# Kernel tuning notes

Hardware: AMD Instinct MI355X
Metric: run time of the kernel (lower is better)

The kernel has to match this reference:

```python
import jax, jax.numpy as jnp
import numpy as np

# AWLoss config (matches init_kwargs): method='fft', filter_dim=2, filter_scale=2,
# mode='reverse', reduction='sum', epsilon=1e-9 (pre-whitening), std=1e-4, eta=0, gamma=0
EPSILON = 1e-9
STD = 1e-4
DIMS = (-2, -1)          # self.dims for filter_dim=2
FS = (3, 511, 511)       # get_filter_shape([B,3,256,256]): [nc, 2H-1, 2W-1]


def pad_signal(x, shape):
    # center-pad dims 1.. of x up to `shape` (extra sample on the right).
    pads = [(0, 0)]
    for i, s in enumerate(shape):
        p1 = (s - x.shape[i + 1]) // 2
        pads.append((p1, s - x.shape[i + 1] - p1))
    return jnp.pad(x, pads)


def make_penalty(shape, std):
    # inverted multivariate gaussian on [-1,1]^d grid: 0 at center, ->1 away
    axes = [jnp.linspace(-1.0, 1.0, n) for n in shape]
    mesh = jnp.stack(jnp.meshgrid(*axes, indexing='ij'), axis=-1)  # (h, w, 2)
    d = mesh.shape[-1]
    logp = -0.5 * jnp.sum((mesh / std) ** 2, axis=-1) \
           - 0.5 * d * jnp.log(2.0 * jnp.pi * std * std)
    rv = jnp.exp(logp)
    rv = rv / jnp.max(jnp.abs(rv))
    return -rv + jnp.max(rv)  # eta=0 => no random additive term


def wienerfft(x, y, fs, prwh):
    # least-squares Wiener filter transforming x into y, via FFT
    Fx_flip = jnp.fft.fftn(jnp.flip(x, DIMS), axes=DIMS)
    Fccorr = Fx_flip * jnp.fft.fftn(y, axes=DIMS)   # cross-correlation spectrum
    Facorr = Fx_flip * jnp.fft.fftn(x, axes=DIMS)   # auto-correlation spectrum
    Fdconv = (Fccorr + prwh) / (Facorr + prwh)      # regularized deconvolution
    # irfftn crops last axis to fs[-1]//2+1 (numpy/torch semantics match)
    rolled = jnp.fft.irfftn(Fdconv, s=fs[-2:], axes=DIMS)
    # roll: int(-n/2)-1 per trailing dim (n odd => -(n//2)-1)
    shifts = tuple(-(x.shape[i] // 2) - 1 for i in range(1, x.ndim))[-2:]
    return jnp.roll(rolled, shifts, axis=DIMS)


def awloss(recon, target):
    fs = FS
    recon_p = pad_signal(recon, fs)   # [B, C, 511, 511]
    target_p = pad_signal(target, fs)
    # mode='reverse': filter transforms target into recon
    x, y = target_p, recon_p
    v = wienerfft(x, y, fs, EPSILON)                       # [B, C, 511, 511]
    vnorm = jnp.sqrt(jnp.sum(v * v, axis=DIMS, keepdims=True))
    v = v / vnorm                                          # unit-energy filter
    T = make_penalty(fs[-2:], STD)                         # (511, 511)
    f = 0.5 * jnp.sum((T * v) ** 2)                        # reduction='sum'
    return f


def setup_inputs() -> dict:
    key = jax.random.key(0)
    k1, k2 = jax.random.split(key)
    recon = jax.random.normal(k1, (16, 3, 256, 256), dtype=jnp.float32)
    target = jax.random.normal(k2, (16, 3, 256, 256), dtype=jnp.float32)
    return {"recon": recon, "target": target}


def reference(recon, target):
    return awloss(recon, target)
```

## Files before the change

### kernel.cpp

```cpp
#include <hip/hip_runtime.h>
#include <math.h>


#define NCH 48
#define PADOFF 127
#define TWO_PI_F 6.283185307179586f

typedef float f32x4 __attribute__((ext_vector_type(4)));
typedef short s16x8 __attribute__((ext_vector_type(8)));
typedef unsigned short u16;

typedef __attribute__((address_space(1))) const unsigned char* gas_p;
typedef __attribute__((address_space(3))) unsigned char* las_p;

union frag_u { u16 u[8]; s16x8 v; };

__device__ __forceinline__ u16 f2bf(float f) {
    union { float f; unsigned u; } x; x.f = f;
    unsigned r = x.u + 0x7FFFu + ((x.u >> 16) & 1u);
    return (u16)(r >> 16);
}

#define MFMA16(A, B, C) __builtin_amdgcn_mfma_f32_16x16x32_bf16(A, B, C, 0, 0, 0)

__global__ __launch_bounds__(256) void setup(u16* __restrict__ w2f,
                                             float* __restrict__ sacc) {
    __shared__ float cs[511], sn[511];
    int tid = threadIdx.x;
    for (int i = tid; i < 511; i += 256) {
        float a = -TWO_PI_F * (float)i / 511.0f;
        cs[i] = cosf(a);
        sn[i] = sinf(a);
    }
    __syncthreads();

    int i = blockIdx.x * 256 + tid;
    int j = i & 7, l = (i >> 3) & 63, kk = (i >> 9) & 7;
    int c = (i >> 12) & 1, kt = i >> 13;
    int k1 = 16 * kt + (l & 15);
    u16 v = 0;
    if (k1 < 511) {
        int n = 32 * kk + 8 * (l >> 4) + j;
        int p = (k1 * (n + PADOFF)) % 511;
        v = f2bf(c ? sn[p] : cs[p]);
    }
    w2f[i] = v;
    if (blockIdx.x == 0 && tid < 2 * NCH) sacc[tid] = 0.0f;
}

__global__ __launch_bounds__(256, 2) void stage1(const float* __restrict__ target,
                                                 const float* __restrict__ recon,
                                                 const u16* __restrict__ w2f,
                                                 u16* __restrict__ x1t,
                                                 int c0) {
    int tid = threadIdx.x;
    int w = tid >> 6, l = tid & 63;
    int lm = l & 15, lh = l >> 4;
    int h   = blockIdx.x & 1;
    int q   = (blockIdx.x >> 1) & 3;
    int imgl = blockIdx.x >> 3;
    int lc = imgl >> 1;
    int tsel = imgl & 1;
    const float* src = (tsel == 0 ? target : recon) + (size_t)(c0 + lc) * 65536;
    int r0 = 64 * q;

    __shared__ u16 lin[16384];

    {
        int row = tid >> 2;
        int cg  = tid & 3;
        const float* rp = src + (size_t)(r0 + row) * 256 + cg * 64;
        float4 v[16];
        #pragma unroll
        for (int i = 0; i < 16; ++i) v[i] = *(const float4*)(rp + 4 * i);
        u16 b[64];
        #pragma unroll
        for (int i = 0; i < 16; ++i) {
            b[4*i]   = f2bf(v[i].x); b[4*i+1] = f2bf(v[i].y);
            b[4*i+2] = f2bf(v[i].z); b[4*i+3] = f2bf(v[i].w);
        }
        int s = row >> 4, lmw = row & 15;
        #pragma unroll
        for (int i2 = 0; i2 < 8; ++i2) {
            int col0 = cg * 64 + i2 * 8;
            int kk = col0 >> 5, lhw = (col0 >> 3) & 3;
            u16* dst = &lin[((s * 8 + kk) * 512) + (lhw * 16 + lmw) * 8];
            *(s16x8*)dst = *(const s16x8*)&b[i2 * 8];
        }
    }

    int t0 = 8 * h + 2 * w;
    s16x8 tw00[8], tw01[8], tw10[8], tw11[8];
    {
        const u16* p0 = w2f + (size_t)t0 * 8192 + l * 8;
        const u16* p1 = w2f + (size_t)(t0 + 1) * 8192 + l * 8;
        #pragma unroll
        for (int kk = 0; kk < 8; ++kk) {
            tw00[kk] = *(const s16x8*)(p0 + kk * 512);
            tw01[kk] = *(const s16x8*)(p0 + 4096 + kk * 512);
            tw10[kk] = *(const s16x8*)(p1 + kk * 512);
            tw11[kk] = *(const s16x8*)(p1 + 4096 + kk * 512);
        }
    }
    __syncthreads();

    f32x4 a00[4], a01[4], a10[4], a11[4];
    #pragma unroll
    for (int s = 0; s < 4; ++s) {
        a00[s] = (f32x4){0,0,0,0}; a01[s] = (f32x4){0,0,0,0};
        a10[s] = (f32x4){0,0,0,0}; a11[s] = (f32x4){0,0,0,0};
    }
    #pragma unroll
    for (int kk = 0; kk < 8; ++kk) {
        s16x8 af[4];
        #pragma unroll
        for (int s = 0; s < 4; ++s)
            af[s] = *(const s16x8*)&lin[((s * 8 + kk) * 512) + l * 8];
        #pragma unroll
        for (int s = 0; s < 4; ++s) {
            a00[s] = MFMA16(af[s], tw00[kk], a00[s]);
            a01[s] = MFMA16(af[s], tw01[kk], a01[s]);
            a10[s] = MFMA16(af[s], tw10[kk], a10[s]);
            a11[s] = MFMA16(af[s], tw11[kk], a11[s]);
        }
    }

    u16* chdst = x1t + (size_t)(lc * 4 + tsel * 2) * 65536;
    #pragma unroll
    for (int s = 0; s < 4; ++s) {
        size_t off0 = (size_t)(16 * t0 + lm) * 256 + r0 + 16 * s + 4 * lh;
        size_t off1 = off0 + 4096;
        ushort4 o;
        o.x = f2bf(a00[s][0]); o.y = f2bf(a00[s][1]);
        o.z = f2bf(a00[s][2]); o.w = f2bf(a00[s][3]);
        *(ushort4*)(chdst + off0) = o;
        o.x = f2bf(a01[s][0]); o.y = f2bf(a01[s][1]);
        o.z = f2bf(a01[s][2]); o.w = f2bf(a01[s][3]);
        *(ushort4*)(chdst + 65536 + off0) = o;
        o.x = f2bf(a10[s][0]); o.y = f2bf(a10[s][1]);
        o.z = f2bf(a10[s][2]); o.w = f2bf(a10[s][3]);
        *(ushort4*)(chdst + off1) = o;
        o.x = f2bf(a11[s][0]); o.y = f2bf(a11[s][1]);
        o.z = f2bf(a11[s][2]); o.w = f2bf(a11[s][3]);
        *(ushort4*)(chdst + 65536 + off1) = o;
    }
}

__global__ __launch_bounds__(256, 2) void stage2(const u16* __restrict__ x1t,
                                                 const u16* __restrict__ w2f,
                                                 float* __restrict__ sacc,
                                                 int c0, int cc) {
    int tid = threadIdx.x;
    int w = tid >> 6, l = tid & 63;
    int lm = l & 15, lh = l >> 4;
    int t   = blockIdx.x & 15;
    int o   = (blockIdx.x >> 4) & 3;
    int chg = blockIdx.x >> 6;
    int ch0 = chg * 6;
    int nch = cc - ch0; if (nch > 6) nch = 6;
    if (nch <= 0) return;

    __shared__ u16 sbufA[16384];
    __shared__ u16 sbufB[16384];
    __shared__ float red[4][12];

    int kt0 = 8 * o + 2 * w;
    s16x8 twr0[8], twi0[8], twr1[8], twi1[8];
    {
        const u16* p0 = w2f + (size_t)kt0 * 8192 + l * 8;
        const u16* p1 = w2f + (size_t)(kt0 + 1) * 8192 + l * 8;
        #pragma unroll
        for (int kk = 0; kk < 8; ++kk) {
            twr0[kk] = *(const s16x8*)(p0 + kk * 512);
            twi0[kk] = *(const s16x8*)(p0 + 4096 + kk * 512);
            twr1[kk] = *(const s16x8*)(p1 + kk * 512);
            twi1[kk] = *(const s16x8*)(p1 + 4096 + kk * 512);
        }
    }

    int k2 = 16 * t + lm;
    float wgt = (k2 == 0) ? 1.f : 2.f;
    int rowoff = (16 * t + lm) * 256 + 8 * lh;
    float s1a[6] = {0,0,0,0,0,0}, s2a[6] = {0,0,0,0,0,0};

#define STAGE(BUF, LC) do {                                                   \
    const u16* cb_ = x1t + (size_t)(4 * (LC)) * 65536;                        \
    _Pragma("unroll")                                                         \
    for (int q = 0; q < 8; ++q) {                                             \
        int pair_ = w * 8 + q;                                                \
        int p_ = pair_ >> 3, kk_ = pair_ & 7;                                 \
        const u16* g_ = cb_ + (size_t)p_ * 65536 + rowoff + 32 * kk_;         \
        __builtin_amdgcn_global_load_lds((gas_p)g_,                           \
            (las_p)&BUF[pair_ * 512], 16, 0, 0);                              \
    } } while (0)

#define COMPUTE(BUF, I) do {                                                  \
    f32x4 c0rr = {0,0,0,0}, c0ii = {0,0,0,0}, c0ri = {0,0,0,0}, c0ir = {0,0,0,0}; \
    f32x4 d0rr = {0,0,0,0}, d0ii = {0,0,0,0}, d0ri = {0,0,0,0}, d0ir = {0,0,0,0}; \
    f32x4 c1rr = {0,0,0,0}, c1ii = {0,0,0,0}, c1ri = {0,0,0,0}, c1ir = {0,0,0,0}; \
    f32x4 d1rr = {0,0,0,0}, d1ii = {0,0,0,0}, d1ri = {0,0,0,0}, d1ir = {0,0,0,0}; \
    _Pragma("unroll")                                                         \
    for (int kk = 0; kk < 8; ++kk) {                                          \
        const u16* fb = &BUF[kk * 512 + l * 8];                               \
        s16x8 ar = *(const s16x8*)(fb);                                       \
        s16x8 ai = *(const s16x8*)(fb + 4096);                                \
        s16x8 br = *(const s16x8*)(fb + 8192);                                \
        s16x8 bi = *(const s16x8*)(fb + 12288);                               \
        c0rr = MFMA16(twr0[kk], ar, c0rr);                                    \
        c0ii = MFMA16(twi0[kk], ai, c0ii);                                    \
        c0ri = MFMA16(twr0[kk], ai, c0ri);                                    \
        c0ir = MFMA16(twi0[kk], ar, c0ir);                                    \
        d0rr = MFMA16(twr0[kk], br, d0rr);                                    \
        d0ii = MFMA16(twi0[kk], bi, d0ii);                                    \
        d0ri = MFMA16(twr0[kk], bi, d0ri);                                    \
        d0ir = MFMA16(twi0[kk], br, d0ir);                                    \
        c1rr = MFMA16(twr1[kk], ar, c1rr);                                    \
        c1ii = MFMA16(twi1[kk], ai, c1ii);                                    \
        c1ri = MFMA16(twr1[kk], ai, c1ri);                                    \
        c1ir = MFMA16(twi1[kk], ar, c1ir);                                    \
        d1rr = MFMA16(twr1[kk], br, d1rr);                                    \
        d1ii = MFMA16(twi1[kk], bi, d1ii);                                    \
        d1ri = MFMA16(twr1[kk], bi, d1ri);                                    \
        d1ir = MFMA16(twi1[kk], br, d1ir);                                    \
    }                                                                         \
    _Pragma("unroll")                                                         \
    for (int r = 0; r < 4; ++r) {                                             \
        {                                                                     \
            float Xr = c0rr[r] - c0ii[r], Xi = c0ri[r] + c0ir[r];             \
            float Yr = d0rr[r] - d0ii[r], Yi = d0ri[r] + d0ir[r];             \
            float Pr = Xr * Yr + Xi * Yi;                                     \
            float Pi = Xr * Yi - Xi * Yr;                                     \
            float Q  = Xr * Xr + Xi * Xi;                                     \
            float inv = 1.0f / (Q * Q + 1e-30f);                              \
            s1a[I] += wgt * Pr * Q * inv;                                     \
            s2a[I] += wgt * (Pr * Pr + Pi * Pi) * inv;                        \
        }                                                                     \
        {                                                                     \
            int k1 = 16 * (kt0 + 1) + 4 * lh + r;                             \
            float wg2 = (k1 < 511) ? wgt : 0.f;                               \
            float Xr = c1rr[r] - c1ii[r], Xi = c1ri[r] + c1ir[r];             \
            float Yr = d1rr[r] - d1ii[r], Yi = d1ri[r] + d1ir[r];             \
            float Pr = Xr * Yr + Xi * Yi;                                     \
            float Pi = Xr * Yi - Xi * Yr;                                     \
            float Q  = Xr * Xr + Xi * Xi;                                     \
            float inv = 1.0f / (Q * Q + 1e-30f);                              \
            s1a[I] += wg2 * Pr * Q * inv;                                     \
            s2a[I] += wg2 * (Pr * Pr + Pi * Pi) * inv;                        \
        }                                                                     \
    } } while (0)

    STAGE(sbufA, ch0);
    __syncthreads();

    #pragma unroll
    for (int i = 0; i < 6; i += 2) {
        if (i >= nch) break;
        if (i + 1 < nch) STAGE(sbufB, ch0 + i + 1);
        COMPUTE(sbufA, i);
        __syncthreads();
        if (i + 1 < nch) {
            if (i + 2 < nch) STAGE(sbufA, ch0 + i + 2);
            COMPUTE(sbufB, i + 1);
            __syncthreads();
        }
    }
#undef STAGE
#undef COMPUTE

    #pragma unroll
    for (int i = 0; i < 6; ++i) {
        #pragma unroll
        for (int off = 32; off > 0; off >>= 1) {
            s1a[i] += __shfl_down(s1a[i], off);
            s2a[i] += __shfl_down(s2a[i], off);
        }
    }
    if (l == 0) {
        #pragma unroll
        for (int i = 0; i < 6; ++i) {
            red[w][2 * i]     = s1a[i];
            red[w][2 * i + 1] = s2a[i];
        }
    }
    __syncthreads();
    if (tid < 12) {
        int i = tid >> 1;
        if (i < nch) {
            float v = red[0][tid] + red[1][tid] + red[2][tid] + red[3][tid];
            atomicAdd(&sacc[(tid & 1) * NCH + c0 + ch0 + i], v);
        }
    }
}

__global__ void finalize(const float* __restrict__ s, float* __restrict__ out) {
    int t = threadIdx.x;
    float v = 0.f;
    if (t < NCH) {
        float s1 = s[t], s2 = s[NCH + t];
        v = (s2 != 0.f) ? (s1 * s1) / s2 : 0.f;
    }
    for (int off = 32; off > 0; off >>= 1) v += __shfl_down(v, off);
    if (t == 0) out[0] = 24.0f - 0.5f * v / 261121.0f;
}

extern "C" void kernel_launch(void* const* d_in, const int* in_sizes, int n_in,
                              void* d_out, int out_size, void* d_ws, size_t ws_size,
                              hipStream_t stream) {
    const float* recon  = (const float*)d_in[0];
    const float* target = (const float*)d_in[1];
    float* out = (float*)d_out;
    char* ws = (char*)d_ws;

    const size_t OFF_W2F = 0;
    const size_t OFF_S   = OFF_W2F + 524288;
    const size_t OFF_X1  = OFF_S + 512;

    u16*   w2f  = (u16*)(ws + OFF_W2F);
    float* sacc = (float*)(ws + OFF_S);
    u16*   x1t  = (u16*)(ws + OFF_X1);

    const size_t perch = 4ull * 65536 * 2;
    size_t avail = (ws_size > OFF_X1) ? ws_size - OFF_X1 : 0;
    int chunk = (int)(avail / perch);
    if (chunk > NCH) chunk = NCH;
    if (chunk < 1) chunk = 1;

    setup<<<dim3(1024), dim3(256), 0, stream>>>(w2f, sacc);

    for (int c0 = 0; c0 < NCH; c0 += chunk) {
        int cc = (NCH - c0 < chunk) ? (NCH - c0) : chunk;
        int ngrp = (cc + 5) / 6;
        stage1<<<dim3(16 * cc), dim3(256), 0, stream>>>(target, recon, w2f, x1t, c0);
        stage2<<<dim3(64 * ngrp), dim3(256), 0, stream>>>(x1t, w2f, sacc, c0, cc);
    }
    finalize<<<dim3(1), dim3(64), 0, stream>>>(sacc, out);
}
```

Measured before the change: 61.25 us.

## Swap stage2 operand residency: keep data tiles in registers, stream twiddles via LDS

Stage2 now keeps each warp's data fragments (real and imaginary parts of both signals) in registers and streams the twiddle-factor tiles through double-buffered LDS. Previously the twiddles were register-resident and the data was staged through LDS. Each warp handles one channel/row-tile task over 8 k-tiles, which raises the block count and drops the per-block channel grouping and shared reduction. In exchange there are more atomics, one per warp, and the register-pressure profile changes because the launch-bounds occupancy hint is removed.

```diff
diff --git a/kernel.cpp b/kernel.cpp
--- a/kernel.cpp
+++ b/kernel.cpp
@@ -146,149 +146,100 @@
     }
 }
 
-__global__ __launch_bounds__(256, 2) void stage2(const u16* __restrict__ x1t,
-                                                 const u16* __restrict__ w2f,
-                                                 float* __restrict__ sacc,
-                                                 int c0, int cc) {
+__global__ __launch_bounds__(256) void stage2(const u16* __restrict__ x1t,
+                                              const u16* __restrict__ w2f,
+                                              float* __restrict__ sacc,
+                                              int c0, int cc) {
     int tid = threadIdx.x;
     int w = tid >> 6, l = tid & 63;
     int lm = l & 15, lh = l >> 4;
-    int t   = blockIdx.x & 15;
-    int o   = (blockIdx.x >> 4) & 3;
-    int chg = blockIdx.x >> 6;
-    int ch0 = chg * 6;
-    int nch = cc - ch0; if (nch > 6) nch = 6;
-    if (nch <= 0) return;
-
-    __shared__ u16 sbufA[16384];
-    __shared__ u16 sbufB[16384];
-    __shared__ float red[4][12];
-
-    int kt0 = 8 * o + 2 * w;
-    s16x8 twr0[8], twi0[8], twr1[8], twi1[8];
-    {
-        const u16* p0 = w2f + (size_t)kt0 * 8192 + l * 8;
-        const u16* p1 = w2f + (size_t)(kt0 + 1) * 8192 + l * 8;
-        #pragma unroll
-        for (int kk = 0; kk < 8; ++kk) {
-            twr0[kk] = *(const s16x8*)(p0 + kk * 512);
-            twi0[kk] = *(const s16x8*)(p0 + 4096 + kk * 512);
-            twr1[kk] = *(const s16x8*)(p1 + kk * 512);
-            twi1[kk] = *(const s16x8*)(p1 + 4096 + kk * 512);
-        }
+    int ktq = blockIdx.x & 3;
+    int grp = blockIdx.x >> 2;
+    int task = grp * 4 + w;
+    int lc = task >> 4;
+    int t  = task & 15;
+
+    __shared__ u16 twA[8192];
+    __shared__ u16 twB[8192];
+
+    const u16* base = x1t + (size_t)(4 * lc) * 65536;
+    int roff = (16 * t + lm) * 256 + 8 * lh;
+    s16x8 ar[8], ai[8], br[8], bi[8];
+    #pragma unroll
+    for (int kk = 0; kk < 8; ++kk) {
+        int off = roff + 32 * kk;
+        ar[kk] = *(const s16x8*)(base + off);
+        ai[kk] = *(const s16x8*)(base + 65536 + off);
+        br[kk] = *(const s16x8*)(base + 131072 + off);
+        bi[kk] = *(const s16x8*)(base + 196608 + off);
     }
 
     int k2 = 16 * t + lm;
     float wgt = (k2 == 0) ? 1.f : 2.f;
-    int rowoff = (16 * t + lm) * 256 + 8 * lh;
-    float s1a[6] = {0,0,0,0,0,0}, s2a[6] = {0,0,0,0,0,0};
-
-#define STAGE(BUF, LC) do {                                                   \
-    const u16* cb_ = x1t + (size_t)(4 * (LC)) * 65536;                        \
+    float s1 = 0.f, s2 = 0.f;
+    int kt0 = 8 * ktq;
+
+#define STAGE_TW(BUF, KT) do {                                                \
+    const u16* gt_ = w2f + (size_t)(KT) * 8192 + (size_t)(w * 64 + l) * 8;    \
     _Pragma("unroll")                                                         \
-    for (int q = 0; q < 8; ++q) {                                             \
-        int pair_ = w * 8 + q;                                                \
-        int p_ = pair_ >> 3, kk_ = pair_ & 7;                                 \
-        const u16* g_ = cb_ + (size_t)p_ * 65536 + rowoff + 32 * kk_;         \
-        __builtin_amdgcn_global_load_lds((gas_p)g_,                           \
-            (las_p)&BUF[pair_ * 512], 16, 0, 0);                              \
+    for (int q_ = 0; q_ < 4; ++q_) {                                          \
+        __builtin_amdgcn_global_load_lds((gas_p)(gt_ + q_ * 2048),            \
+            (las_p)&BUF[(q_ * 256 + w * 64) * 8], 16, 0, 0);                  \
     } } while (0)
 
-#define COMPUTE(BUF, I) do {                                                  \
-    f32x4 c0rr = {0,0,0,0}, c0ii = {0,0,0,0}, c0ri = {0,0,0,0}, c0ir = {0,0,0,0}; \
-    f32x4 d0rr = {0,0,0,0}, d0ii = {0,0,0,0}, d0ri = {0,0,0,0}, d0ir = {0,0,0,0}; \
-    f32x4 c1rr = {0,0,0,0}, c1ii = {0,0,0,0}, c1ri = {0,0,0,0}, c1ir = {0,0,0,0}; \
-    f32x4 d1rr = {0,0,0,0}, d1ii = {0,0,0,0}, d1ri = {0,0,0,0}, d1ir = {0,0,0,0}; \
+#define COMPUTE(BUF, KT) do {                                                 \
+    f32x4 crr = {0,0,0,0}, cii = {0,0,0,0}, cri = {0,0,0,0}, cir = {0,0,0,0}; \
+    f32x4 drr = {0,0,0,0}, dii = {0,0,0,0}, dri = {0,0,0,0}, dir = {0,0,0,0}; \
     _Pragma("unroll")                                                         \
     for (int kk = 0; kk < 8; ++kk) {                                          \
-        const u16* fb = &BUF[kk * 512 + l * 8];                               \
-        s16x8 ar = *(const s16x8*)(fb);                                       \
-        s16x8 ai = *(const s16x8*)(fb + 4096);                                \
-        s16x8 br = *(const s16x8*)(fb + 8192);                                \
-        s16x8 bi = *(const s16x8*)(fb + 12288);                               \
-        c0rr = MFMA16(twr0[kk], ar, c0rr);                                    \
-        c0ii = MFMA16(twi0[kk], ai, c0ii);                                    \
-        c0ri = MFMA16(twr0[kk], ai, c0ri);                                    \
-        c0ir = MFMA16(twi0[kk], ar, c0ir);                                    \
-        d0rr = MFMA16(twr0[kk], br, d0rr);                                    \
-        d0ii = MFMA16(twi0[kk], bi, d0ii);                                    \
-        d0ri = MFMA16(twr0[kk], bi, d0ri);                                    \
-        d0ir = MFMA16(twi0[kk], br, d0ir);                                    \
-        c1rr = MFMA16(twr1[kk], ar, c1rr);                                    \
-        c1ii = MFMA16(twi1[kk], ai, c1ii);                                    \
-        c1ri = MFMA16(twr1[kk], ai, c1ri);                                    \
-        c1ir = MFMA16(twi1[kk], ar, c1ir);                                    \
-        d1rr = MFMA16(twr1[kk], br, d1rr);                                    \
-        d1ii = MFMA16(twi1[kk], bi, d1ii);                                    \
-        d1ri = MFMA16(twr1[kk], bi, d1ri);                                    \
-        d1ir = MFMA16(twi1[kk], br, d1ir);                                    \
+        s16x8 wr = *(const s16x8*)&BUF[kk * 512 + l * 8];                     \
+        s16x8 wi = *(const s16x8*)&BUF[4096 + kk * 512 + l * 8];              \
+        crr = MFMA16(wr, ar[kk], crr);                                        \
+        cii = MFMA16(wi, ai[kk], cii);                                        \
+        cri = MFMA16(wr, ai[kk], cri);                                        \
+        cir = MFMA16(wi, ar[kk], cir);                                        \
+        drr = MFMA16(wr, br[kk], drr);                                        \
+        dii = MFMA16(wi, bi[kk], dii);                                        \
+        dri = MFMA16(wr, bi[kk], dri);                                        \
+        dir = MFMA16(wi, br[kk], dir);                                        \
     }                                                                         \
     _Pragma("unroll")                                                         \
     for (int r = 0; r < 4; ++r) {                                             \
-        {                                                                     \
-            float Xr = c0rr[r] - c0ii[r], Xi = c0ri[r] + c0ir[r];             \
-            float Yr = d0rr[r] - d0ii[r], Yi = d0ri[r] + d0ir[r];             \
-            float Pr = Xr * Yr + Xi * Yi;                                     \
-            float Pi = Xr * Yi - Xi * Yr;                                     \
-            float Q  = Xr * Xr + Xi * Xi;                                     \
-            float inv = 1.0f / (Q * Q + 1e-30f);                              \
-            s1a[I] += wgt * Pr * Q * inv;                                     \
-            s2a[I] += wgt * (Pr * Pr + Pi * Pi) * inv;                        \
-        }                                                                     \
-        {                                                                     \
-            int k1 = 16 * (kt0 + 1) + 4 * lh + r;                             \
-            float wg2 = (k1 < 511) ? wgt : 0.f;                               \
-            float Xr = c1rr[r] - c1ii[r], Xi = c1ri[r] + c1ir[r];             \
-            float Yr = d1rr[r] - d1ii[r], Yi = d1ri[r] + d1ir[r];             \
-            float Pr = Xr * Yr + Xi * Yi;                                     \
-            float Pi = Xr * Yi - Xi * Yr;                                     \
-            float Q  = Xr * Xr + Xi * Xi;                                     \
-            float inv = 1.0f / (Q * Q + 1e-30f);                              \
-            s1a[I] += wg2 * Pr * Q * inv;                                     \
-            s2a[I] += wg2 * (Pr * Pr + Pi * Pi) * inv;                        \
-        }                                                                     \
+        int k1 = 16 * (KT) + 4 * lh + r;                                      \
+        float wg2 = (k1 < 511) ? wgt : 0.f;                                   \
+        float Xr = crr[r] - cii[r], Xi = cri[r] + cir[r];                     \
+        float Yr = drr[r] - dii[r], Yi = dri[r] + dir[r];                     \
+        float Pr = Xr * Yr + Xi * Yi;                                         \
+        float Pi = Xr * Yi - Xi * Yr;                                         \
+        float Q  = Xr * Xr + Xi * Xi;                                         \
+        float inv = 1.0f / (Q * Q + 1e-30f);                                  \
+        s1 += wg2 * Pr * Q * inv;                                             \
+        s2 += wg2 * (Pr * Pr + Pi * Pi) * inv;                                \
     } } while (0)
 
-    STAGE(sbufA, ch0);
+    STAGE_TW(twA, kt0);
     __syncthreads();
 
     #pragma unroll
-    for (int i = 0; i < 6; i += 2) {
-        if (i >= nch) break;
-        if (i + 1 < nch) STAGE(sbufB, ch0 + i + 1);
-        COMPUTE(sbufA, i);
+    for (int i8 = 0; i8 < 8; i8 += 2) {
+        STAGE_TW(twB, kt0 + i8 + 1);
+        COMPUTE(twA, kt0 + i8);
         __syncthreads();
-        if (i + 1 < nch) {
-            if (i + 2 < nch) STAGE(sbufA, ch0 + i + 2);
-            COMPUTE(sbufB, i + 1);
-            __syncthreads();
-        }
-    }
-#undef STAGE
+        if (i8 + 2 < 8) STAGE_TW(twA, kt0 + i8 + 2);
+        COMPUTE(twB, kt0 + i8 + 1);
+        __syncthreads();
+    }
+#undef STAGE_TW
 #undef COMPUTE
 
     #pragma unroll
-    for (int i = 0; i < 6; ++i) {
-        #pragma unroll
-        for (int off = 32; off > 0; off >>= 1) {
-            s1a[i] += __shfl_down(s1a[i], off);
-            s2a[i] += __shfl_down(s2a[i], off);
-        }
+    for (int off = 32; off > 0; off >>= 1) {
+        s1 += __shfl_down(s1, off);
+        s2 += __shfl_down(s2, off);
     }
     if (l == 0) {
-        #pragma unroll
-        for (int i = 0; i < 6; ++i) {
-            red[w][2 * i]     = s1a[i];
-            red[w][2 * i + 1] = s2a[i];
-        }
-    }
-    __syncthreads();
-    if (tid < 12) {
-        int i = tid >> 1;
-        if (i < nch) {
-            float v = red[0][tid] + red[1][tid] + red[2][tid] + red[3][tid];
-            atomicAdd(&sacc[(tid & 1) * NCH + c0 + ch0 + i], v);
-        }
+        atomicAdd(&sacc[c0 + lc], s1);
+        atomicAdd(&sacc[NCH + c0 + lc], s2);
     }
 }
 
@@ -329,9 +280,8 @@
 
     for (int c0 = 0; c0 < NCH; c0 += chunk) {
         int cc = (NCH - c0 < chunk) ? (NCH - c0) : chunk;
-        int ngrp = (cc + 5) / 6;
         stage1<<<dim3(16 * cc), dim3(256), 0, stream>>>(target, recon, w2f, x1t, c0);
-        stage2<<<dim3(64 * ngrp), dim3(256), 0, stream>>>(x1t, w2f, sacc, c0, cc);
+        stage2<<<dim3(16 * cc), dim3(256), 0, stream>>>(x1t, w2f, sacc, c0, cc);
     }
     finalize<<<dim3(1), dim3(64), 0, stream>>>(sacc, out);
 }
```

Result: slower. 86.21 us (+40.8%).
